# Optimization experiments

Hardware: AMD Instinct MI355X
Metric: run time of the kernel (lower is better)

Reference implementation:

```python
import jax, jax.numpy as jnp
import numpy as np

WIN = 15
BINS = 32
ALPHA = 0.9
LAM1 = 0.5
LAM2 = 0.5


def _tmedian(x, axis):
    # torch-style median: k-th smallest with k=(n-1)//2 (lower middle), keepdims
    n = x.shape[axis]
    s = jnp.sort(x, axis=axis)
    return jnp.take(s, jnp.array([(n - 1) // 2]), axis=axis)


def _box_sum_1d(x, k, axis):
    # sliding-window sum (zero padding) via cumsum / integral image
    p = k // 2
    L = x.shape[axis]
    c = jnp.cumsum(x, axis=axis)
    pad = [(0, 0)] * x.ndim
    pad[axis] = (1, 0)
    c = jnp.pad(c, pad)
    i = jnp.arange(L)
    hi = jnp.clip(i + p + 1, 0, L)
    lo = jnp.clip(i - p, 0, L)
    return jnp.take(c, hi, axis=axis) - jnp.take(c, lo, axis=axis)


def _counts_1d(L, k, dtype):
    p = k // 2
    i = jnp.arange(L)
    return (jnp.clip(i + p + 1, 0, L) - jnp.clip(i - p, 0, L)).astype(dtype)


def box_avg(x, k):
    # avg_pool2d(stride=1, padding=k//2, count_include_pad=False) on [B,C,H,W]
    s = _box_sum_1d(_box_sum_1d(x, k, 2), k, 3)
    c = _counts_1d(x.shape[2], k, x.dtype)[:, None] * _counts_1d(x.shape[3], k, x.dtype)[None, :]
    return s / c


def avg3(x):
    # avg_pool2d(k=3, stride=1, pad=1, count_include_pad=True)
    return _box_sum_1d(_box_sum_1d(x, 3, 2), 3, 3) / 9.0


def _softplus(x):
    t = jnp.log1p(jnp.exp(-jnp.abs(x)))
    return jnp.where(x >= 0, x + t, t)


def _conv3(x, k):
    return jax.lax.conv_general_dilated(x, k, (1, 1), ((1, 1), (1, 1)),
                                        dimension_numbers=('NCHW', 'OIHW', 'NCHW'))


def _forward(lab, a_rand):
    B, _, H, W = lab.shape
    N = H * W
    f32 = lab.dtype
    L = lab[:, 0:1]
    a = lab[:, 1:2]
    b = lab[:, 2:3]
    kx = jnp.array([[-1, 0, 1], [-2, 0, 2], [-1, 0, 1]], f32).reshape(1, 1, 3, 3)
    ky = jnp.array([[-1, -2, -1], [0, 0, 0], [1, 2, 1]], f32).reshape(1, 1, 3, 3)
    gx = _conv3(L, kx)
    gy = _conv3(L, ky)
    E = avg3(gx * gx) + avg3(gy * gy)           # structure-tensor trace
    S = jnp.sqrt(a * a + b * b + 1e-8)           # chroma
    Xf = jnp.concatenate([E, S], 1).reshape(B, 2, N).transpose(0, 2, 1)   # [B,N,2]
    yf = L.reshape(B, 1, N).transpose(0, 2, 1)                            # [B,N,1]
    XtX = jnp.einsum('bni,bnj->bij', Xf, Xf)
    XtY = jnp.einsum('bni,bnj->bij', Xf, yf)
    beta = jnp.linalg.solve(XtX + 1e-6 * jnp.eye(2, dtype=f32), XtY)[..., 0]  # [B,2]
    pred = beta[:, 0][:, None, None, None] * E + beta[:, 1][:, None, None, None] * S
    L_perp = L - pred
    # robust scale + whitening of [L_perp, E, S]
    X3f = jnp.concatenate([L_perp, E, S], 1).reshape(B, 3, N).transpose(0, 2, 1)  # [B,N,3]
    med = _tmedian(X3f, 1)
    mad = _tmedian(jnp.abs(X3f - med), 1) * 1.4826 + 1e-8
    Xz = (X3f - med) / mad
    diff = Xz - Xz.mean(1, keepdims=True)
    cov = jnp.einsum('bni,bnj->bij', diff, diff) / N
    e, V = jnp.linalg.eigh(jnp.maximum(cov, 1e-8))
    Wwh = jnp.einsum('bij,bj,bkj->bik', V, 1.0 / jnp.sqrt(e), V)
    Xw = diff @ Wwh                                                       # [B,N,3]
    # 128-way random-projection kurtosis search
    an = a_rand / (jnp.linalg.norm(a_rand, axis=-1, keepdims=True) + 1e-12)
    z = jnp.einsum('bni,bti->bnt', Xw, an)                                # [B,N,128]
    zc = z - z.mean(1, keepdims=True)
    m2 = (zc ** 2).mean(1) + 1e-12
    m4 = (zc ** 4).mean(1)
    kurt = m4 / (m2 * m2) - 3.0
    best = jnp.argmax(jnp.abs(kurt), axis=1)
    a_star = jnp.take_along_axis(an, best[:, None, None], axis=1)[:, 0]   # [B,3]
    z_best = jnp.einsum('bni,bi->bn', Xw, a_star)                         # [B,N]
    # 1-D 2-component GMM, 10 EM steps
    K = 2
    q25 = jnp.quantile(z_best, 0.25, axis=1)
    q75 = jnp.quantile(z_best, 0.75, axis=1)
    mu = jnp.stack([q25, q75], 1)[:, None, :]   # [B,1,K]
    var = jnp.ones((B, 1, K), f32)
    pi = jnp.full((B, 1, K), 0.5, f32)
    x1 = z_best[:, :, None]                      # [B,N,1]
    R = jnp.zeros((B, N, K), f32)
    for _ in range(10):
        logp = (-0.5 * ((x1 - mu) ** 2 / (var + 1e-6))
                - 0.5 * jnp.log(var + 1e-6) + jnp.log(pi + 1e-8))
        R = jnp.exp(jax.nn.log_softmax(logp, axis=2))
        Nk = R.sum(1, keepdims=True)             # [B,1,K]
        mu = (R * x1).sum(1, keepdims=True) / (Nk + 1e-8)
        var = (R * (x1 - mu) ** 2).sum(1, keepdims=True) / (Nk + 1e-8) + 1e-6
        pi = Nk / N
    R_alpha = R ** ALPHA
    R_alpha = R_alpha / (R_alpha.sum(2, keepdims=True) + 1e-8)
    rk_maps = R_alpha.transpose(0, 2, 1).reshape(B, K, 1, H, W)
    # per-cluster weighted Mahalanobis distance in [L_perp,E,S] space
    eye3 = jnp.eye(3, dtype=f32)
    Dk = []
    for k in range(K):
        w = R_alpha[:, :, k]
        Wsum = w.sum(1, keepdims=True) + 1e-8
        mu_k = jnp.einsum('bn,bni->bi', w, X3f) / Wsum
        Xm = X3f - mu_k[:, None, :]
        cov_k = jnp.einsum('bn,bni,bnj->bij', w, Xm, Xm) / Wsum[..., None] + 1e-6 * eye3
        inv_k = jnp.linalg.inv(cov_k)
        Dk.append(jnp.sqrt(jnp.einsum('bni,bij,bnj->bn', Xm, inv_k, Xm) + 1e-8))
    Dk = jnp.stack(Dk, 2)                        # [B,N,K]
    Rtemp = jax.nn.softmax(jnp.log(R_alpha + 1e-8), axis=2)
    D_M = (Rtemp * Dk).sum(2).reshape(B, 1, H, W)
    # local luminance anomaly (box-filtered weighted mean/std)
    Z_LLA = []
    for k in range(K):
        rk = rk_maps[:, k]
        den = box_avg(rk, WIN) + 1e-8
        mu_b = box_avg(rk * L_perp, WIN) / den
        var_b = jnp.maximum(box_avg(rk * L_perp ** 2, WIN) / den - mu_b ** 2, 1e-8)
        lla = jnp.abs(L_perp - mu_b) / (jnp.sqrt(var_b) + 1e-8)
        v = lla.reshape(B, 1, N)
        mv = _tmedian(v, 2)
        mdv = _tmedian(jnp.abs(v - mv), 2) * 1.4826 + 1e-8
        Z_LLA.append(((v - mv) / mdv).reshape(B, 1, H, W))
    # global-vs-local histogram distance (GLD)
    Lmin = L_perp.min(axis=(2, 3), keepdims=True)
    Lmax = L_perp.max(axis=(2, 3), keepdims=True)
    Lnorm = jnp.clip((L_perp - Lmin) / (Lmax - Lmin + 1e-8), 0, 1)
    idx = jnp.clip((Lnorm * BINS).astype(jnp.int32), 0, BINS - 1)[:, 0]   # [B,H,W]
    onehot = jax.nn.one_hot(idx, BINS, dtype=f32).transpose(0, 3, 1, 2)   # [B,bins,H,W]
    Z_GLD = []
    for k in range(K):
        rk = rk_maps[:, k]
        w_hist = onehot * rk
        g_hist = w_hist.reshape(B, BINS, N).sum(-1)
        g_hist = g_hist / (g_hist.sum(1, keepdims=True) + 1e-8)
        g_cdf = jnp.cumsum(g_hist, 1)
        loc_cdf = jnp.cumsum(box_avg(w_hist, WIN), 1) / (box_avg(rk, WIN) + 1e-8)
        GLD = jnp.abs(loc_cdf - g_cdf[:, :, None, None]).sum(1) / BINS    # [B,H,W]
        v = GLD.reshape(B, N)
        mv = _tmedian(v, 1)                                              # [B,1]
        mdv = _tmedian(jnp.abs(v - mv), 1) * 1.4826 + 1e-8
        Z_GLD.append(((GLD - mv[:, :, None]) / mdv[:, :, None])[:, None])
    gamma = jnp.ones_like(L_perp)
    for k in range(K):
        gamma = gamma + rk_maps[:, k] * (LAM1 * _softplus(Z_LLA[k]) + LAM2 * _softplus(Z_GLD[k]))
    # structural decorrelation term over [E,S]
    ES = jnp.concatenate([E, S], 1).reshape(B, 2, N).transpose(0, 2, 1)
    med2 = _tmedian(ES, 1)
    mad2 = _tmedian(jnp.abs(ES - med2), 1) * 1.4826 + 1e-8
    ESz = (ES - med2) / mad2
    d = ESz - ESz.mean(1, keepdims=True)
    cov2 = jnp.einsum('bni,bnj->bij', d, d) / N + 1e-6 * jnp.eye(2, dtype=f32)
    inv2 = jnp.linalg.inv(cov2)
    d2 = jnp.einsum('bni,bij,bnj->bn', d, inv2, d).reshape(B, 1, H, W)
    R_struct = jnp.exp(-0.5 * d2)
    L_anom = jnp.maximum(D_M * gamma * (1.0 - R_struct), 0.0)
    flat = L_anom.reshape(B, -1)
    q1 = jnp.quantile(flat, 0.01, axis=1).reshape(B, 1, 1, 1)
    q9 = jnp.quantile(flat, 0.99, axis=1).reshape(B, 1, 1, 1)
    L_anom_norm = jnp.clip((L_anom - q1) / (q9 - q1 + 1e-8), 0, 1)
    return L_perp, L_anom_norm


def setup_inputs() -> dict:
    key = jax.random.key(0)
    k1, k2 = jax.random.split(key)
    return {
        'batch_lab_raw': jax.random.normal(k1, (2, 3, 384, 384), jnp.float32),
        'a_rand': jax.random.normal(k2, (2, 128, 3), jnp.float32),
    }


def reference(batch_lab_raw, a_rand):
    return _forward(batch_lab_raw, a_rand)
```

## Files before the change

kernel.cpp:

```cpp
#include <hip/hip_runtime.h>
#include <math.h>

#define HH 384
#define WW 384
#define NPIX (HH*WW)
#define NB 2
#define BN (NB*NPIX)
#define NT 128
#define NBINS 32
#define MEDRANK ((NPIX-1)/2)
#define RB 72
#define RB2 288
#define SEL_BLK 64
#define KDG 8
#define KSEG 16

#define A_BETA 0
#define A_XZ   16
#define A_ES   40
#define A_DK   56
#define A_GMM  128
#define A_ZTOT 272
#define A_GHIST 288
#define A_KURT 512

#define F_BETA 0
#define F_X3   8
#define F_MEAN 24
#define F_WWH  32
#define F_ASTAR 828
#define F_ZBQ  868
#define F_DKINV 880
#define F_LLA  918
#define F_GLD  924
#define F_ESI  940
#define F_LAQ  952
#define F_GCDF 968
#define F_MMS_MIN 1280
#define F_MMS_MAX 1408


__device__ __forceinline__ double waveSum(double v){
#pragma unroll
  for(int o=32;o;o>>=1) v += __shfl_down(v,o,64);
  return v;
}
__device__ __forceinline__ unsigned f2u(float f){
  unsigned u = __float_as_uint(f);
  return (u & 0x80000000u) ? ~u : (u | 0x80000000u);
}
__device__ __forceinline__ float u2f(unsigned u){
  return __uint_as_float((u & 0x80000000u) ? (u ^ 0x80000000u) : ~u);
}
__device__ __forceinline__ float sp(float x){
  float t = log1pf(expf(-fabsf(x)));
  return x >= 0.f ? x + t : t;
}

struct SelBatch {
  const float* src[8];
  int rank[8];
  int fslot[8];
  int nt;
  int medmad;
};

__device__ void pickN(const unsigned* hp, int nb, int rank, unsigned& sel, int& nrank){
  __shared__ unsigned s_cum[256];
  __shared__ unsigned s_res[2];
  int tid = threadIdx.x;
  int base = tid*8;
  unsigned loc[8]; unsigned tsum=0;
#pragma unroll
  for(int j=0;j<8;j++){ unsigned v=(base+j<nb)?hp[base+j]:0u; loc[j]=v; tsum+=v; }
  s_cum[tid]=tsum;
  __syncthreads();
  for(int o=1;o<256;o<<=1){
    unsigned t=(tid>=o)?s_cum[tid-o]:0u;
    __syncthreads();
    s_cum[tid]+=t;
    __syncthreads();
  }
  unsigned cum=s_cum[tid], ex=cum-tsum;
  if(tsum>0u && (unsigned)rank>=ex && (unsigned)rank<cum){
    int rr=rank-(int)ex; unsigned bsel=0;
#pragma unroll
    for(int j=0;j<8;j++){ if((unsigned)rr<loc[j]){ bsel=(unsigned)(base+j); break; } rr-=(int)loc[j]; }
    s_res[0]=bsel; s_res[1]=(unsigned)rr;
  }
  __syncthreads();
  sel=s_res[0]; nrank=(int)s_res[1];
  __syncthreads();
}

__global__ void k_zero(double* A, float* F, unsigned* T, unsigned* H){
  int i = blockIdx.x*256 + threadIdx.x;
  if(i < 2048) A[i] = 0.0;
  if(i < 4096){
    unsigned* U = (unsigned*)F;
    unsigned v = 0u;
    if(i>=F_MMS_MIN && i<F_MMS_MIN+64) v = 0xFFFFFFFFu;
    U[i] = v;
  }
  if(i < 512) T[i] = 0u;
  for(int j=i; j<240*2048; j+=65536) H[j]=0u;
}

__global__ __launch_bounds__(256) void k_selp(SelBatch sb, unsigned* Hh, unsigned* T,
                                              float* F, int bid, int stage, int p){
  int task = blockIdx.x / SEL_BLK;
  int blk  = blockIdx.x % SEL_BLK;
  unsigned* meta = T + 384 + task*8;
  float center = (stage==1) ? __uint_as_float(meta[4]) : 0.f;
  unsigned pre = (p==2) ? 0u : meta[stage*2];
  __shared__ unsigned lh[2048];
  for(int j=threadIdx.x;j<2048;j+=256) lh[j]=0u;
  __syncthreads();
  const float* src = sb.src[task];
  for(int i=blk*256+threadIdx.x; i<NPIX; i+=SEL_BLK*256){
    float v = src[i];
    if(stage) v = fabsf(v-center);
    unsigned u = f2u(v);
    unsigned bin; bool ok;
    if(p==2){ bin = u>>21; ok = true; }
    else if(p==1){ bin = (u>>10)&2047u; ok = ((u>>21)==pre); }
    else { bin = u&1023u; ok = ((u>>10)==pre); }
    if(ok) atomicAdd(&lh[bin],1u);
  }
  __syncthreads();
  unsigned* hp = Hh + (size_t)(((bid*8+task)*2+stage)*3 + (2-p))*2048;
  for(int j=threadIdx.x;j<2048;j+=256){ unsigned c=lh[j]; if(c) atomicAdd(hp+j,c); }
  __shared__ int s_last;
  __syncthreads();
  if(threadIdx.x==0){
    __threadfence();
    s_last = (atomicAdd(&T[16+bid*64+task*8+stage*4+(2-p)],1u) == (unsigned)(SEL_BLK-1));
  }
  __syncthreads();
  if(!s_last) return;
  int r = (p==2) ? sb.rank[task] : (int)meta[stage*2+1];
  int nb = (p==0) ? 1024 : 2048;
  unsigned sel; int nr;
  pickN(hp, nb, r, sel, nr);
  if(threadIdx.x==0){
    if(p==2){ meta[stage*2]=sel; meta[stage*2+1]=(unsigned)nr; }
    else if(p==1){ meta[stage*2]=(pre<<11)|sel; meta[stage*2+1]=(unsigned)nr; }
    else {
      float val = u2f((pre<<10)|sel);
      if(stage==0){
        if(sb.medmad) meta[4]=__float_as_uint(val);
        else F[sb.fslot[task]]=val;
      } else {
        F[sb.fslot[task]]   = __uint_as_float(meta[4]);
        F[sb.fslot[task]+1] = val*1.4826f + 1e-8f;
      }
    }
  }
}

__device__ void quad_from_stats(double N0,double Sx0,double Sxx0,double Sxt,double Sxxt,
                                float& qa,float& qb,float& qc){
  double Nt=(double)NPIX;
  double N1=Nt-N0, Sx1=Sxt-Sx0, Sxx1=Sxxt-Sxx0;
  double mu0=Sx0/(N0+1e-8), mu1=Sx1/(N1+1e-8);
  double v0=(Sxx0-2.0*mu0*Sx0+mu0*mu0*N0)/(N0+1e-8)+1e-6;
  double v1=(Sxx1-2.0*mu1*Sx1+mu1*mu1*N1)/(N1+1e-8)+1e-6;
  double p0=N0/Nt, p1=N1/Nt;
  double c0=-0.5*log(v0+1e-6)+log(p0+1e-8);
  double c1=-0.5*log(v1+1e-6)+log(p1+1e-8);
  double iv0=0.5/(v0+1e-6), iv1=0.5/(v1+1e-6);
  qa=(float)(iv0-iv1);
  qb=(float)(2.0*(iv1*mu1-iv0*mu0));
  qc=(float)(iv0*mu0*mu0-iv1*mu1*mu1+c1-c0);
}
__device__ void quad_init(const float* F,int b,float& qa,float& qb,float& qc){
  const float* z = F + F_ZBQ + b*4;
  double h25 = 0.25*(double)(NPIX-1); double f25 = h25 - floor(h25);
  double h75 = 0.75*(double)(NPIX-1); double f75 = h75 - floor(h75);
  double mu0 = (double)z[0] + f25*((double)z[1]-(double)z[0]);
  double mu1 = (double)z[2] + f75*((double)z[3]-(double)z[2]);
  double iv = 0.5/(1.0+1e-6);
  qa = 0.f;
  qb = (float)(2.0*iv*(mu1-mu0));
  qc = (float)(iv*(mu0*mu0-mu1*mu1));
}

__global__ __launch_bounds__(256) void k_sobel(const float* lab, float* S, float* E){
  int bx = blockIdx.x % 24, by = (blockIdx.x/24) % 24, b = blockIdx.x/576;
  __shared__ float Lt[20][21];
  __shared__ float G[18][19];
  const float* Lb = lab + b*3*NPIX;
  int ox = bx*16, oy = by*16;
  for(int i=threadIdx.x; i<400; i+=256){
    int lx=i%20, ly=i/20;
    int gx_=ox-2+lx, gy_=oy-2+ly;
    Lt[ly][lx] = (gx_<0||gx_>=WW||gy_<0||gy_>=HH)?0.f:Lb[gy_*WW+gx_];
  }
  __syncthreads();
  for(int i=threadIdx.x; i<324; i+=256){
    int lx=i%18, ly=i/18;
    int px=lx+1, py=ly+1;
    int gxp=ox-2+px, gyp=oy-2+py;
    float g=0.f;
    if(gxp>=0&&gxp<WW&&gyp>=0&&gyp<HH){
      float gx = -Lt[py-1][px-1]+Lt[py-1][px+1] -2.f*Lt[py][px-1]+2.f*Lt[py][px+1] -Lt[py+1][px-1]+Lt[py+1][px+1];
      float gy = -Lt[py-1][px-1]-2.f*Lt[py-1][px]-Lt[py-1][px+1] +Lt[py+1][px-1]+2.f*Lt[py+1][px]+Lt[py+1][px+1];
      g = gx*gx+gy*gy;
    }
    G[ly][lx]=g;
  }
  __syncthreads();
  int tx = threadIdx.x%16, ty = threadIdx.x/16;
  float s=0;
#pragma unroll
  for(int dy=0;dy<3;dy++)
#pragma unroll
    for(int dx=0;dx<3;dx++) s += G[ty+dy][tx+dx];
  int n = (oy+ty)*WW + ox+tx;
  E[b*NPIX+n] = s*(1.f/9.f);
  float av=Lb[NPIX+n], bv=Lb[2*NPIX+n];
  S[b*NPIX+n] = sqrtf(av*av+bv*bv+1e-8f);
}

__global__ void k_beta_red(const float* E,const float* S,const float* lab,double* A,
                           float* F, unsigned* T){
  int b = blockIdx.x / RB, blk = blockIdx.x % RB;
  double s[5]={0,0,0,0,0};
  for(int n = blk*256 + threadIdx.x; n < NPIX; n += RB*256){
    float e=E[b*NPIX+n], ss=S[b*NPIX+n], l=lab[b*3*NPIX+n];
    s[0]+=(double)e*e; s[1]+=(double)e*ss; s[2]+=(double)ss*ss;
    s[3]+=(double)e*l; s[4]+=(double)ss*l;
  }
  __shared__ double red[4][5];
  int wave=threadIdx.x>>6, lane=threadIdx.x&63;
#pragma unroll
  for(int q=0;q<5;q++){
    s[q]=waveSum(s[q]);
    if(lane==0) red[wave][q]=s[q];
  }
  __syncthreads();
  if(threadIdx.x<5){
    double v = red[0][threadIdx.x]+red[1][threadIdx.x]+red[2][threadIdx.x]+red[3][threadIdx.x];
    atomicAdd(&A[A_BETA+b*5+threadIdx.x], v);
  }
  __shared__ int s_last;
  __syncthreads();
  if(threadIdx.x==0){
    __threadfence();
    s_last = (atomicAdd(&T[0],1u) == (unsigned)(NB*RB-1));
  }
  __syncthreads();
  if(!s_last || threadIdx.x) return;
  for(int bb=0;bb<NB;bb++){
    double EE=A[A_BETA+bb*5],ES=A[A_BETA+bb*5+1],SS=A[A_BETA+bb*5+2],EL=A[A_BETA+bb*5+3],SL=A[A_BETA+bb*5+4];
    double a00=EE+1e-6, a01=ES, a11=SS+1e-6;
    double det=a00*a11-a01*a01;
    F[F_BETA+bb*2]  =(float)(( a11*EL - a01*SL)/det);
    F[F_BETA+bb*2+1]=(float)((-a01*EL + a00*SL)/det);
  }
}

__global__ void k_lperp(const float* lab,const float* E,const float* S,const float* F,float* out0){
  int i = blockIdx.x*256 + threadIdx.x;
  int b=i/NPIX, n=i%NPIX;
  float v = lab[b*3*NPIX+n] - F[F_BETA+b*2]*E[i] - F[F_BETA+b*2+1]*S[i];
  out0[i] = v;
  unsigned u = f2u(v);
  unsigned mn=u, mx=u;
#pragma unroll
  for(int o=32;o;o>>=1){
    unsigned a = __shfl_down(mn,o,64); mn = (a<mn)?a:mn;
    unsigned c = __shfl_down(mx,o,64); mx = (c>mx)?c:mx;
  }
  __shared__ unsigned rmn[4], rmx[4];
  int wave=threadIdx.x>>6, lane=threadIdx.x&63;
  if(lane==0){ rmn[wave]=mn; rmx[wave]=mx; }
  __syncthreads();
  if(threadIdx.x==0){
    unsigned m0 = rmn[0]; unsigned m1 = rmx[0];
    for(int w=1;w<4;w++){ if(rmn[w]<m0)m0=rmn[w]; if(rmx[w]>m1)m1=rmx[w]; }
    unsigned* U = (unsigned*)F;
    int slot = blockIdx.x & 31;
    atomicMin(&U[F_MMS_MIN+b*32+slot], m0);
    atomicMax(&U[F_MMS_MAX+b*32+slot], m1);
  }
}

__global__ void k_xz_red(const float* Lp,const float* E,const float* S,float* F,double* A,
                         unsigned* T){
  int b = blockIdx.x / RB, blk = blockIdx.x % RB;
  const float* M = F + F_X3 + b*6;
  double s[9]={0,0,0,0,0,0,0,0,0};
  for(int n = blk*256 + threadIdx.x; n < NPIX; n += RB*256){
    float z0=(Lp[b*NPIX+n]-M[0])/M[1];
    float z1=(E [b*NPIX+n]-M[2])/M[3];
    float z2=(S [b*NPIX+n]-M[4])/M[5];
    s[0]+=z0; s[1]+=z1; s[2]+=z2;
    s[3]+=(double)z0*z0; s[4]+=(double)z0*z1; s[5]+=(double)z0*z2;
    s[6]+=(double)z1*z1; s[7]+=(double)z1*z2; s[8]+=(double)z2*z2;
  }
  __shared__ double red[4][9];
  int wave=threadIdx.x>>6, lane=threadIdx.x&63;
#pragma unroll
  for(int q=0;q<9;q++){
    s[q]=waveSum(s[q]);
    if(lane==0) red[wave][q]=s[q];
  }
  __syncthreads();
  if(threadIdx.x<9){
    double v = red[0][threadIdx.x]+red[1][threadIdx.x]+red[2][threadIdx.x]+red[3][threadIdx.x];
    atomicAdd(&A[A_XZ+b*9+threadIdx.x], v);
  }
  __shared__ int s_last;
  __syncthreads();
  if(threadIdx.x==0){
    __threadfence();
    s_last = (atomicAdd(&T[1],1u) == (unsigned)(NB*RB-1));
  }
  __syncthreads();
  if(!s_last) return;
  int bb = threadIdx.x;
  if(bb>=NB) return;
  const double* ss = A + A_XZ + bb*9;
  double inv = 1.0/(double)NPIX;
  double m0=ss[0]*inv, m1=ss[1]*inv, m2=ss[2]*inv;
  double a[3][3];
  a[0][0]=fmax(ss[3]*inv-m0*m0,1e-8);
  a[0][1]=a[1][0]=fmax(ss[4]*inv-m0*m1,1e-8);
  a[0][2]=a[2][0]=fmax(ss[5]*inv-m0*m2,1e-8);
  a[1][1]=fmax(ss[6]*inv-m1*m1,1e-8);
  a[1][2]=a[2][1]=fmax(ss[7]*inv-m1*m2,1e-8);
  a[2][2]=fmax(ss[8]*inv-m2*m2,1e-8);
  double V[3][3]={{1,0,0},{0,1,0},{0,0,1}};
  for(int sweep=0;sweep<40;sweep++){
    for(int pp=0;pp<3;pp++){
      int p = (pp==2)?1:0;
      int q = (pp==0)?1:2;
      double apq=a[p][q];
      if(fabs(apq)<1e-30) continue;
      double theta=(a[q][q]-a[p][p])/(2.0*apq);
      double t=((theta>=0)?1.0:-1.0)/(fabs(theta)+sqrt(1.0+theta*theta));
      double c=1.0/sqrt(1.0+t*t), sn=t*c;
      for(int k2=0;k2<3;k2++){ double akp=a[k2][p],akq=a[k2][q];
        a[k2][p]=c*akp-sn*akq; a[k2][q]=sn*akp+c*akq; }
      for(int k2=0;k2<3;k2++){ double apk=a[p][k2],aqk=a[q][k2];
        a[p][k2]=c*apk-sn*aqk; a[q][k2]=sn*apk+c*aqk; }
      for(int k2=0;k2<3;k2++){ double vkp=V[k2][p],vkq=V[k2][q];
        V[k2][p]=c*vkp-sn*vkq; V[k2][q]=sn*vkp+c*vkq; }
    }
  }
  double is0=1.0/sqrt(a[0][0]), is1=1.0/sqrt(a[1][1]), is2=1.0/sqrt(a[2][2]);
  for(int i=0;i<3;i++) for(int j=0;j<3;j++){
    double w = V[i][0]*is0*V[j][0] + V[i][1]*is1*V[j][1] + V[i][2]*is2*V[j][2];
    F[F_WWH + bb*9 + i*3 + j] = (float)w;
  }
  F[F_MEAN+bb*3]=(float)m0; F[F_MEAN+bb*3+1]=(float)m1; F[F_MEAN+bb*3+2]=(float)m2;
}

__global__ void k_xw(const float* Lp,const float* E,const float* S,const float* F,
                     float* Xw,int* idxP){
  __shared__ float s_mn, s_mx;
  int i = blockIdx.x*256 + threadIdx.x;
  int b=i/NPIX;
  if(threadIdx.x==0){
    const unsigned* U = (const unsigned*)F;
    unsigned mn=0xFFFFFFFFu, mx=0u;
    for(int s2=0;s2<32;s2++){
      unsigned a=U[F_MMS_MIN+b*32+s2]; if(a<mn)mn=a;
      unsigned c=U[F_MMS_MAX+b*32+s2]; if(c>mx)mx=c;
    }
    s_mn=u2f(mn); s_mx=u2f(mx);
  }
  __syncthreads();
  const float* M = F + F_X3 + b*6;
  float lp = Lp[i];
  float z0=(lp-M[0])/M[1];
  float z1=(E [i]-M[2])/M[3];
  float z2=(S [i]-M[4])/M[5];
  float d0=z0-F[F_MEAN+b*3], d1=z1-F[F_MEAN+b*3+1], d2=z2-F[F_MEAN+b*3+2];
  const float* Wm = F + F_WWH + b*9;
  Xw[3*(size_t)i  ]=d0*Wm[0]+d1*Wm[3]+d2*Wm[6];
  Xw[3*(size_t)i+1]=d0*Wm[1]+d1*Wm[4]+d2*Wm[7];
  Xw[3*(size_t)i+2]=d0*Wm[2]+d1*Wm[5]+d2*Wm[8];
  float ln = (lp-s_mn)/(s_mx-s_mn+1e-8f);
  ln = fminf(fmaxf(ln,0.f),1.f);
  int id = (int)(ln*32.f);
  idxP[i] = id>31?31:(id<0?0:id);
}

__global__ __launch_bounds__(256) void k_kurt(const float* Xw, const float* arand, double* A){
  int g = blockIdx.x;
  int b   = g / ((NT/KDG)*KSEG);
  int rem = g % ((NT/KDG)*KSEG);
  int dg  = rem / KSEG;
  int seg = rem % KSEG;
  float a0[KDG],a1[KDG],a2[KDG];
#pragma unroll
  for(int j=0;j<KDG;j++){
    const float* ar = arand + (b*NT+dg*KDG+j)*3;
    float q0=ar[0],q1=ar[1],q2=ar[2];
    float nrm=(float)(sqrt((double)q0*q0+(double)q1*q1+(double)q2*q2)+1e-12);
    a0[j]=q0/nrm; a1[j]=q1/nrm; a2[j]=q2/nrm;
  }
  const float* X = Xw + (size_t)b*NPIX*3;
  double s[KDG][4];
#pragma unroll
  for(int j=0;j<KDG;j++){ s[j][0]=0; s[j][1]=0; s[j][2]=0; s[j][3]=0; }
  const int cnt = NPIX/KSEG;
  int start = seg*cnt;
  for(int n=start+threadIdx.x; n<start+cnt; n+=256){
    const float* p = X + 3*(size_t)n;
    float x=p[0], y=p[1], z=p[2];
#pragma unroll
    for(int j=0;j<KDG;j++){
      float zz = fmaf(x,a0[j],fmaf(y,a1[j], z*a2[j]));
      float z2f = zz*zz;
      s[j][0]+=zz; s[j][1]+=z2f; s[j][2]+=z2f*zz; s[j][3]+=(double)z2f*z2f;
    }
  }
  __shared__ double red[4][KDG*4];
  int wave=threadIdx.x>>6, lane=threadIdx.x&63;
#pragma unroll
  for(int j=0;j<KDG;j++)
#pragma unroll
    for(int m=0;m<4;m++){
      double v=waveSum(s[j][m]);
      if(lane==0) red[wave][j*4+m]=v;
    }
  __syncthreads();
  if(threadIdx.x<KDG*4){
    double v = red[0][threadIdx.x]+red[1][threadIdx.x]+red[2][threadIdx.x]+red[3][threadIdx.x];
    int j=threadIdx.x>>2, m=threadIdx.x&3;
    atomicAdd(&A[A_KURT + (size_t)(b*NT+dg*KDG+j)*4 + m], v);
  }
}
__global__ void k_kurt_pick(const double* A, const float* arand, float* F){
  int b = blockIdx.x;
  int t = threadIdx.x;
  __shared__ float ak[NT];
  const double* K = A + A_KURT + (size_t)(b*NT+t)*4;
  double inv=1.0/(double)NPIX;
  double mean=K[0]*inv, M2=K[1]*inv, M3=K[2]*inv, M4=K[3]*inv;
  double m2 = M2 - mean*mean + 1e-12;
  double m4 = M4 - 4.0*mean*M3 + 6.0*mean*mean*M2 - 3.0*mean*mean*mean*mean;
  ak[t] = (float)fabs(m4/(m2*m2) - 3.0);
  __syncthreads();
  if(t==0){
    int best=0; float bv=ak[0];
    for(int j=1;j<NT;j++) if(ak[j]>bv){bv=ak[j];best=j;}
    const float* ar = arand + (b*NT+best)*3;
    double nrm = sqrt((double)ar[0]*ar[0]+(double)ar[1]*ar[1]+(double)ar[2]*ar[2])+1e-12;
    F[F_ASTAR+b*3]  =(float)(ar[0]/nrm);
    F[F_ASTAR+b*3+1]=(float)(ar[1]/nrm);
    F[F_ASTAR+b*3+2]=(float)(ar[2]/nrm);
  }
}
__global__ void k_zbest(const float* Xw,const float* F,float* zb,double* A){
  int i = blockIdx.x*256 + threadIdx.x;
  int b=i/NPIX;
  const float* p = Xw + 3*(size_t)i;
  float v = p[0]*F[F_ASTAR+b*3] + p[1]*F[F_ASTAR+b*3+1] + p[2]*F[F_ASTAR+b*3+2];
  zb[i]=v;
  double s0=waveSum((double)v), s1=waveSum((double)v*v);
  __shared__ double red[4][2];
  int wave=threadIdx.x>>6, lane=threadIdx.x&63;
  if(lane==0){ red[wave][0]=s0; red[wave][1]=s1; }
  __syncthreads();
  if(threadIdx.x<2){
    double v2 = red[0][threadIdx.x]+red[1][threadIdx.x]+red[2][threadIdx.x]+red[3][threadIdx.x];
    atomicAdd(&A[A_ZTOT+b*2+threadIdx.x], v2);
  }
}

__global__ __launch_bounds__(256) void k_gmm_red(const float* zb, const float* F, double* A, int it){
  __shared__ float Q[3];
  __shared__ double red[4][3];
  int b = blockIdx.x / RB2, blk = blockIdx.x % RB2;
  if(threadIdx.x==0){
    float qa,qb,qc;
    if(it==0) quad_init(F,b,qa,qb,qc);
    else {
      const double* g = A + A_GMM + (it-1)*8 + b*4;
      quad_from_stats(g[0],g[1],g[2],A[A_ZTOT+b*2],A[A_ZTOT+b*2+1],qa,qb,qc);
    }
    Q[0]=qa;Q[1]=qb;Q[2]=qc;
  }
  __syncthreads();
  float qa=Q[0],qb=Q[1],qc=Q[2];
  double s0=0,s1=0,s2=0;
  for(int n = blk*256 + threadIdx.x; n < NPIX; n += RB2*256){
    float x = zb[b*NPIX+n];
    float f = fmaf(fmaf(qa,x,qb),x,qc);
    float r0 = 1.f/(1.f+expf(f));
    float rx = r0*x;
    s0+=r0; s1+=rx; s2+=(double)rx*x;
  }
  int wave=threadIdx.x>>6, lane=threadIdx.x&63;
  s0=waveSum(s0); s1=waveSum(s1); s2=waveSum(s2);
  if(lane==0){ red[wave][0]=s0; red[wave][1]=s1; red[wave][2]=s2; }
  __syncthreads();
  if(threadIdx.x<3){
    double v = red[0][threadIdx.x]+red[1][threadIdx.x]+red[2][threadIdx.x]+red[3][threadIdx.x];
    atomicAdd(&A[A_GMM+it*8+b*4+threadIdx.x], v);
  }
}

__global__ void k_ralpha(const float* zb, float* F, double* A, const int* idxP,
                         float* Ra0, float* Ra1, unsigned* T){
  __shared__ float h0[NBINS], h1[NBINS];
  __shared__ float Q[3];
  if(threadIdx.x<NBINS){ h0[threadIdx.x]=0.f; h1[threadIdx.x]=0.f; }
  int i = blockIdx.x*256 + threadIdx.x;
  int b=i/NPIX;
  if(threadIdx.x==0){
    const double* g = A + A_GMM + 8*8 + b*4;
    float qa,qb,qc;
    quad_from_stats(g[0],g[1],g[2],A[A_ZTOT+b*2],A[A_ZTOT+b*2+1],qa,qb,qc);
    Q[0]=qa;Q[1]=qb;Q[2]=qc;
  }
  __syncthreads();
  float x = zb[i];
  float f = fmaf(fmaf(Q[0],x,Q[1]),x,Q[2]);
  float r0 = 1.f/(1.f+expf(f));
  float r1 = 1.f-r0;
  float ra0=powf(r0,0.9f), ra1=powf(r1,0.9f);
  float s=ra0+ra1+1e-8f;
  ra0/=s; ra1/=s;
  Ra0[i]=ra0; Ra1[i]=ra1;
  int id = idxP[i];
  atomicAdd(&h0[id], ra0);
  atomicAdd(&h1[id], ra1);
  __syncthreads();
  if(threadIdx.x<NBINS){
    if(h0[threadIdx.x]!=0.f) atomicAdd(&A[A_GHIST+(0*NB+b)*32+threadIdx.x], (double)h0[threadIdx.x]);
    if(h1[threadIdx.x]!=0.f) atomicAdd(&A[A_GHIST+(1*NB+b)*32+threadIdx.x], (double)h1[threadIdx.x]);
  }
  __shared__ int s_last;
  __syncthreads();
  if(threadIdx.x==0){
    __threadfence();
    s_last = (atomicAdd(&T[2],1u) == (unsigned)(BN/256-1));
  }
  __syncthreads();
  if(!s_last) return;
  int t = threadIdx.x;
  if(t>=4) return;
  const double* gh = A + A_GHIST + t*32;
  double sum=0;
  for(int j=0;j<NBINS;j++) sum += gh[j];
  double c=0;
  for(int j=0;j<NBINS;j++){
    c += gh[j]/(sum+1e-8);
    F[F_GCDF+t*32+j]=(float)c;
  }
}

__global__ void k_dk_red(const float* Lp,const float* E,const float* S,
                         const float* Ra0,const float* Ra1,double* A,float* F,unsigned* T){
  int b = blockIdx.x / RB, blk = blockIdx.x % RB;
  double s[20];
#pragma unroll
  for(int q=0;q<20;q++) s[q]=0;
  for(int n = blk*256 + threadIdx.x; n < NPIX; n += RB*256){
    int i=b*NPIX+n;
    double w0=Ra0[i], w1=Ra1[i];
    double x0=Lp[i], x1=E[i], x2=S[i];
    s[0]+=w0; s[1]+=w0*x0; s[2]+=w0*x1; s[3]+=w0*x2;
    s[4]+=w0*x0*x0; s[5]+=w0*x0*x1; s[6]+=w0*x0*x2; s[7]+=w0*x1*x1; s[8]+=w0*x1*x2; s[9]+=w0*x2*x2;
    s[10]+=w1; s[11]+=w1*x0; s[12]+=w1*x1; s[13]+=w1*x2;
    s[14]+=w1*x0*x0; s[15]+=w1*x0*x1; s[16]+=w1*x0*x2; s[17]+=w1*x1*x1; s[18]+=w1*x1*x2; s[19]+=w1*x2*x2;
  }
  __shared__ double red[4][20];
  int wave=threadIdx.x>>6, lane=threadIdx.x&63;
#pragma unroll
  for(int q=0;q<20;q++){
    s[q]=waveSum(s[q]);
    if(lane==0) red[wave][q]=s[q];
  }
  __syncthreads();
  if(threadIdx.x<20){
    double v = red[0][threadIdx.x]+red[1][threadIdx.x]+red[2][threadIdx.x]+red[3][threadIdx.x];
    atomicAdd(&A[A_DK+b*20+threadIdx.x], v);
  }
  __shared__ int s_last;
  __syncthreads();
  if(threadIdx.x==0){
    __threadfence();
    s_last = (atomicAdd(&T[3],1u) == (unsigned)(NB*RB-1));
  }
  __syncthreads();
  if(!s_last || threadIdx.x) return;
  for(int bb=0;bb<NB;bb++) for(int k=0;k<2;k++){
    const double* ss = A + A_DK + (bb*2+k)*10;
    double W0=ss[0], Ws=W0+1e-8;
    double mu0=ss[1]/Ws, mu1=ss[2]/Ws, mu2=ss[3]/Ws;
    double C00=(ss[4]-2.0*mu0*ss[1]+mu0*mu0*W0)/Ws + 1e-6;
    double C01=(ss[5]-mu0*ss[2]-mu1*ss[1]+mu0*mu1*W0)/Ws;
    double C02=(ss[6]-mu0*ss[3]-mu2*ss[1]+mu0*mu2*W0)/Ws;
    double C11=(ss[7]-2.0*mu1*ss[2]+mu1*mu1*W0)/Ws + 1e-6;
    double C12=(ss[8]-mu1*ss[3]-mu2*ss[2]+mu1*mu2*W0)/Ws;
    double C22=(ss[9]-2.0*mu2*ss[3]+mu2*mu2*W0)/Ws + 1e-6;
    double det = C00*(C11*C22-C12*C12) - C01*(C01*C22-C12*C02) + C02*(C01*C12-C11*C02);
    double id = 1.0/det;
    float* P = F + F_DKINV + (bb*2+k)*9;
    P[0]=(float)((C11*C22-C12*C12)*id);
    P[1]=(float)((C02*C12-C01*C22)*id);
    P[2]=(float)((C01*C12-C02*C11)*id);
    P[3]=(float)((C00*C22-C02*C02)*id);
    P[4]=(float)((C01*C02-C00*C12)*id);
    P[5]=(float)((C00*C11-C01*C01)*id);
    P[6]=(float)mu0; P[7]=(float)mu1; P[8]=(float)mu2;
  }
}
__global__ void k_dm(const float* Lp,const float* E,const float* S,
                     const float* Ra0,const float* Ra1,const float* F,float* DM){
  int i = blockIdx.x*256 + threadIdx.x; if(i>=BN) return;
  int b=i/NPIX;
  float x0=Lp[i], x1=E[i], x2=S[i];
  float D[2];
#pragma unroll
  for(int k=0;k<2;k++){
    const float* P = F + F_DKINV + (b*2+k)*9;
    float d0=x0-P[6], d1=x1-P[7], d2=x2-P[8];
    float q = d0*d0*P[0] + d1*d1*P[3] + d2*d2*P[5]
            + 2.f*(d0*d1*P[1] + d0*d2*P[2] + d1*d2*P[4]);
    D[k]=sqrtf(q+1e-8f);
  }
  float w0=Ra0[i]+1e-8f, w1=Ra1[i]+1e-8f;
  DM[i] = (w0*D[0]+w1*D[1])/(w0+w1);
}

__global__ __launch_bounds__(256) void k_lla(const float* rk, const float* Lp, float* tmpL){
  int bx = blockIdx.x % 24, by = (blockIdx.x/24) % 24, b = blockIdx.x/576;
  __shared__ float Rt[30][31], Lt[30][31];
  __shared__ float h0[30][17], h1[30][17], h2[30][17];
  int ox = bx*16, oy = by*16;
  const float* Rb = rk + (size_t)b*NPIX;
  const float* Lb = Lp + (size_t)b*NPIX;
  for(int i=threadIdx.x; i<900; i+=256){
    int lx=i%30, ly=i/30;
    int gx_=ox-7+lx, gy_=oy-7+ly;
    bool in = (gx_>=0&&gx_<WW&&gy_>=0&&gy_<HH);
    Rt[ly][lx]= in ? Rb[gy_*WW+gx_] : 0.f;
    Lt[ly][lx]= in ? Lb[gy_*WW+gx_] : 0.f;
  }
  __syncthreads();
  for(int i=threadIdx.x; i<480; i+=256){
    int j=i%16, r=i/16;
    float s0=0,s1=0,s2=0;
#pragma unroll
    for(int d=0;d<15;d++){
      float rr=Rt[r][j+d], ll=Lt[r][j+d];
      s0+=rr; float rl=rr*ll; s1+=rl; s2+=rl*ll;
    }
    h0[r][j]=s0; h1[r][j]=s1; h2[r][j]=s2;
  }
  __syncthreads();
  int tx=threadIdx.x%16, ty=threadIdx.x/16;
  float S0=0,S1=0,S2=0;
#pragma unroll
  for(int d=0;d<15;d++){ S0+=h0[ty+d][tx]; S1+=h1[ty+d][tx]; S2+=h2[ty+d][tx]; }
  int x=ox+tx, y=oy+ty;
  float cy = (float)((y+8<HH?y+8:HH)-(y-7>0?y-7:0));
  float cx = (float)((x+8<WW?x+8:WW)-(x-7>0?x-7:0));
  float cnt = cy*cx;
  float den = S0/cnt + 1e-8f;
  float mu  = (S1/cnt)/den;
  float var = fmaxf((S2/cnt)/den - mu*mu, 1e-8f);
  int n = y*WW+x;
  tmpL[b*NPIX+n] = fabsf(Lb[n]-mu)/(sqrtf(var)+1e-8f);
}

__global__ __launch_bounds__(256) void k_gldf(const float* rk, const int* idxP, const float* F,
                                              int k, float* tmpG){
  int bx = blockIdx.x % 24, by = (blockIdx.x/24) % 24, b = blockIdx.x/576;
  __shared__ float Rt[30][31];
  __shared__ unsigned char It[30][32];
  __shared__ float Hh[480*33];
  __shared__ float gc[NBINS];
  if(threadIdx.x<NBINS) gc[threadIdx.x]=F[F_GCDF+(k*NB+b)*32+threadIdx.x];
  int ox=bx*16, oy=by*16;
  const float* Rb = rk + (size_t)b*NPIX;
  const int* Ib = idxP + (size_t)b*NPIX;
  for(int i=threadIdx.x;i<900;i+=256){
    int lx=i%30, ly=i/30;
    int gx_=ox-7+lx, gy_=oy-7+ly;
    bool in = (gx_>=0&&gx_<WW&&gy_>=0&&gy_<HH);
    Rt[ly][lx] = in? Rb[gy_*WW+gx_] : 0.f;
    It[ly][lx] = in? (unsigned char)Ib[gy_*WW+gx_] : 0;
  }
  for(int i=threadIdx.x;i<480*33;i+=256) Hh[i]=0.f;
  __syncthreads();
  for(int i=threadIdx.x;i<480;i+=256){
    int j=i%16, r=i/16;
    float* my = Hh + i*33;
    for(int d=0;d<15;d++) my[It[r][j+d]] += Rt[r][j+d];
  }
  __syncthreads();
  int tx=threadIdx.x%16, ty=threadIdx.x/16;
  float vs[32];
  float tot=0;
#pragma unroll
  for(int bin=0;bin<NBINS;bin++){
    float s=0;
#pragma unroll
    for(int d=0;d<15;d++) s += Hh[((ty+d)*16+tx)*33+bin];
    vs[bin]=s; tot+=s;
  }
  int x=ox+tx, y=oy+ty;
  float cy = (float)((y+8<HH?y+8:HH)-(y-7>0?y-7:0));
  float cx = (float)((x+8<WW?x+8:WW)-(x-7>0?x-7:0));
  float cnt = cy*cx;
  float den = tot/cnt + 1e-8f;
  float cs=0, acc=0;
#pragma unroll
  for(int bin=0;bin<NBINS;bin++){
    cs += vs[bin];
    acc += fabsf((cs/cnt)/den - gc[bin]);
  }
  tmpG[b*NPIX + y*WW + x] = acc*(1.f/32.f);
}

__global__ void k_gamma(const float* tmpL,const float* tmpG,const float* rk,const float* F,
                        float* gamma,int first){
  int i = blockIdx.x*256 + threadIdx.x; if(i>=BN) return;
  int b=i/NPIX;
  float zl=(tmpL[i]-F[F_LLA+b*2])/F[F_LLA+b*2+1];
  float zg=(tmpG[i]-F[F_GLD+b*2])/F[F_GLD+b*2+1];
  float c = rk[i]*(0.5f*sp(zl)+0.5f*sp(zg));
  gamma[i] = first ? 1.0f + c : gamma[i] + c;
}

__global__ void k_es_red(const float* E,const float* S,float* F,double* A,unsigned* T){
  int b = blockIdx.x / RB, blk = blockIdx.x % RB;
  const float* M = F + F_X3 + b*6;
  double s[5]={0,0,0,0,0};
  for(int n = blk*256 + threadIdx.x; n < NPIX; n += RB*256){
    float z0=(E[b*NPIX+n]-M[2])/M[3];
    float z1=(S[b*NPIX+n]-M[4])/M[5];
    s[0]+=z0; s[1]+=z1; s[2]+=(double)z0*z0; s[3]+=(double)z0*z1; s[4]+=(double)z1*z1;
  }
  __shared__ double red[4][5];
  int wave=threadIdx.x>>6, lane=threadIdx.x&63;
#pragma unroll
  for(int q=0;q<5;q++){
    s[q]=waveSum(s[q]);
    if(lane==0) red[wave][q]=s[q];
  }
  __syncthreads();
  if(threadIdx.x<5){
    double v = red[0][threadIdx.x]+red[1][threadIdx.x]+red[2][threadIdx.x]+red[3][threadIdx.x];
    atomicAdd(&A[A_ES+b*5+threadIdx.x], v);
  }
  __shared__ int s_last;
  __syncthreads();
  if(threadIdx.x==0){
    __threadfence();
    s_last = (atomicAdd(&T[4],1u) == (unsigned)(NB*RB-1));
  }
  __syncthreads();
  if(!s_last || threadIdx.x) return;
  for(int bb=0;bb<NB;bb++){
    const double* ss = A + A_ES + bb*5;
    double inv=1.0/(double)NPIX;
    double m0=ss[0]*inv, m1=ss[1]*inv;
    double c00=ss[2]*inv - m0*m0 + 1e-6;
    double c01=ss[3]*inv - m0*m1;
    double c11=ss[4]*inv - m1*m1 + 1e-6;
    double det=c00*c11-c01*c01;
    float* P = F + F_ESI + bb*5;
    P[0]=(float)m0; P[1]=(float)m1;
    P[2]=(float)(c11/det); P[3]=(float)(-c01/det); P[4]=(float)(c00/det);
  }
}
__global__ void k_lanom(const float* E,const float* S,const float* DM,const float* gamma,
                        const float* F,float* La){
  int i = blockIdx.x*256 + threadIdx.x; if(i>=BN) return;
  int b=i/NPIX;
  const float* M = F + F_X3 + b*6;
  const float* P = F + F_ESI + b*5;
  float z0=(E[i]-M[2])/M[3];
  float z1=(S[i]-M[4])/M[5];
  float d0=z0-P[0], d1=z1-P[1];
  float d2 = d0*d0*P[2] + 2.f*d0*d1*P[3] + d1*d1*P[4];
  float Rs = expf(-0.5f*d2);
  La[i] = fmaxf(DM[i]*gamma[i]*(1.f-Rs), 0.f);
}
__global__ void k_out2(const float* La, const float* F, float* out){
  int i = blockIdx.x*256 + threadIdx.x; if(i>=BN) return;
  int b=i/NPIX;
  const float* v = F + F_LAQ + b*4;
  double h1 = 0.01*(double)(NPIX-1); double f1 = h1 - floor(h1);
  double h9 = 0.99*(double)(NPIX-1); double f9 = h9 - floor(h9);
  float q1 = (float)((double)v[0] + f1*((double)v[1]-(double)v[0]));
  float q9 = (float)((double)v[2] + f9*((double)v[3]-(double)v[2]));
  float r = (La[i]-q1)/(q9-q1+1e-8f);
  out[BN + i] = fminf(fmaxf(r,0.f),1.f);
}

static void run_sel(const SelBatch& sb, unsigned* H, unsigned* T, float* F, int bid, hipStream_t s){
  for(int p=2;p>=0;--p) k_selp<<<sb.nt*SEL_BLK,256,0,s>>>(sb,H,T,F,bid,0,p);
  if(sb.medmad) for(int p=2;p>=0;--p) k_selp<<<sb.nt*SEL_BLK,256,0,s>>>(sb,H,T,F,bid,1,p);
}

extern "C" void kernel_launch(void* const* d_in, const int* in_sizes, int n_in,
                              void* d_out, int out_size, void* d_ws, size_t ws_size,
                              hipStream_t stream){
  (void)in_sizes; (void)n_in; (void)out_size; (void)ws_size;
  const float* lab   = (const float*)d_in[0];
  const float* arand = (const float*)d_in[1];
  float* out = (float*)d_out;
  char* wsb = (char*)d_ws;
  double* A = (double*)wsb;
  float*  F = (float*)(wsb + 16384);
  unsigned* T = (unsigned*)(wsb + 32768);
  unsigned* H = (unsigned*)(wsb + 65536);
  float* planes = (float*)(wsb + (size_t)4*1024*1024);
  float* E    = planes;
  float* S    = planes + (size_t)BN;
  float* tA   = planes + (size_t)2*BN;
  float* tmpL = planes + (size_t)5*BN;
  float* tmpG = planes + (size_t)6*BN;
  float* Xw   = planes + (size_t)7*BN;
  float* zb   = planes + (size_t)10*BN;
  float* Ra0  = planes + (size_t)11*BN;
  float* Ra1  = planes + (size_t)12*BN;
  float* DM   = planes + (size_t)13*BN;
  float* gamma= planes + (size_t)14*BN;
  int*   idxP = (int*)(planes + (size_t)16*BN);

  const int GBN = BN/256;

  k_zero<<<256,256,0,stream>>>(A,F,T,H);
  k_sobel<<<NB*576,256,0,stream>>>(lab,S,E);
  k_beta_red<<<NB*RB,256,0,stream>>>(E,S,lab,A,F,T);
  k_lperp<<<GBN,256,0,stream>>>(lab,E,S,F,out);

  SelBatch sbX; sbX.nt=6; sbX.medmad=1;
  for(int b=0;b<NB;b++){
    sbX.src[b*3+0]=out+(size_t)b*NPIX; sbX.src[b*3+1]=E+(size_t)b*NPIX; sbX.src[b*3+2]=S+(size_t)b*NPIX;
    for(int ch=0;ch<3;ch++){ sbX.rank[b*3+ch]=MEDRANK; sbX.fslot[b*3+ch]=F_X3+(b*3+ch)*2; }
  }
  run_sel(sbX,H,T,F,0,stream);

  k_xz_red<<<NB*RB,256,0,stream>>>(out,E,S,F,A,T);
  k_xw<<<GBN,256,0,stream>>>(out,E,S,F,Xw,idxP);
  k_kurt<<<NB*(NT/KDG)*KSEG,256,0,stream>>>(Xw,arand,A);
  k_kurt_pick<<<NB,128,0,stream>>>(A,arand,F);
  k_zbest<<<GBN,256,0,stream>>>(Xw,F,zb,A);

  SelBatch sbZ; sbZ.nt=8; sbZ.medmad=0;
  {
    int rr[4]={36863,36864,110591,110592};
    for(int b=0;b<NB;b++) for(int ri=0;ri<4;ri++){
      int t=b*4+ri;
      sbZ.src[t]=zb+(size_t)b*NPIX; sbZ.rank[t]=rr[ri]; sbZ.fslot[t]=F_ZBQ+b*4+ri;
    }
  }
  run_sel(sbZ,H,T,F,1,stream);

  for(int it=0; it<9; ++it)
    k_gmm_red<<<NB*RB2,256,0,stream>>>(zb,F,A,it);
  k_ralpha<<<GBN,256,0,stream>>>(zb,F,A,idxP,Ra0,Ra1,T);
  k_dk_red<<<NB*RB,256,0,stream>>>(out,E,S,Ra0,Ra1,A,F,T);
  k_dm<<<GBN,256,0,stream>>>(out,E,S,Ra0,Ra1,F,DM);

  SelBatch sbC; sbC.nt=4; sbC.medmad=1;
  for(int b=0;b<NB;b++){
    sbC.src[b]  =tmpL+(size_t)b*NPIX; sbC.rank[b]  =MEDRANK; sbC.fslot[b]  =F_LLA+b*2;
    sbC.src[2+b]=tmpG+(size_t)b*NPIX; sbC.rank[2+b]=MEDRANK; sbC.fslot[2+b]=F_GLD+b*2;
  }

  for(int k=0;k<2;k++){
    const float* Rk = k ? Ra1 : Ra0;
    k_lla<<<NB*576,256,0,stream>>>(Rk,out,tmpL);
    k_gldf<<<NB*576,256,0,stream>>>(Rk,idxP,F,k,tmpG);
    run_sel(sbC,H,T,F,2+k,stream);
    k_gamma<<<GBN,256,0,stream>>>(tmpL,tmpG,Rk,F,gamma,k==0?1:0);
  }

  k_es_red<<<NB*RB,256,0,stream>>>(E,S,F,A,T);
  k_lanom<<<GBN,256,0,stream>>>(E,S,DM,gamma,F,tA);

  SelBatch sbL; sbL.nt=8; sbL.medmad=0;
  {
    int rr[4]={1474,1475,145980,145981};
    for(int b=0;b<NB;b++) for(int ri=0;ri<4;ri++){
      int t=b*4+ri;
      sbL.src[t]=tA+(size_t)b*NPIX; sbL.rank[t]=rr[ri]; sbL.fslot[t]=F_LAQ+b*4+ri;
    }
  }
  run_sel(sbL,H,T,F,4,stream);

  k_out2<<<GBN,256,0,stream>>>(tA,F,out);
}
```

Baseline: 703.3 us.

## Batch both mixture components into single local-stat, selection and gamma launches

Merges the two per-component passes of k_lla/k_gldf into single double-size grids, runs one median/MAD selection over all 8 planes instead of two 4-plane runs, and computes gamma for both components in one kernel. The kurtosis pick is folded into k_kurt with a last-block atomic counter, which removes a separate launch. The GLD shared histogram is transposed to bin-major layout without padding to change bank access patterns. These cut launch count and serialization but use more workspace and require the T[5] counter and the selection slot indices to stay consistent.

```diff
diff --git a/kernel.cpp b/kernel.cpp
--- a/kernel.cpp
+++ b/kernel.cpp
@@ -31,8 +31,7 @@
 #define F_ASTAR 828
 #define F_ZBQ  868
 #define F_DKINV 880
-#define F_LLA  918
-#define F_GLD  924
+#define F_CM   918
 #define F_ESI  940
 #define F_LAQ  952
 #define F_GCDF 968
@@ -388,7 +387,8 @@
   idxP[i] = id>31?31:(id<0?0:id);
 }
 
-__global__ __launch_bounds__(256) void k_kurt(const float* Xw, const float* arand, double* A){
+__global__ __launch_bounds__(256) void k_kurt(const float* Xw, const float* arand,
+                                              double* A, float* F, unsigned* T){
   int g = blockIdx.x;
   int b   = g / ((NT/KDG)*KSEG);
   int rem = g % ((NT/KDG)*KSEG);
@@ -433,28 +433,37 @@
     int j=threadIdx.x>>2, m=threadIdx.x&3;
     atomicAdd(&A[A_KURT + (size_t)(b*NT+dg*KDG+j)*4 + m], v);
   }
-}
-__global__ void k_kurt_pick(const double* A, const float* arand, float* F){
-  int b = blockIdx.x;
-  int t = threadIdx.x;
-  __shared__ float ak[NT];
-  const double* K = A + A_KURT + (size_t)(b*NT+t)*4;
-  double inv=1.0/(double)NPIX;
-  double mean=K[0]*inv, M2=K[1]*inv, M3=K[2]*inv, M4=K[3]*inv;
-  double m2 = M2 - mean*mean + 1e-12;
-  double m4 = M4 - 4.0*mean*M3 + 6.0*mean*mean*M2 - 3.0*mean*mean*mean*mean;
-  ak[t] = (float)fabs(m4/(m2*m2) - 3.0);
-  __syncthreads();
-  if(t==0){
-    int best=0; float bv=ak[0];
-    for(int j=1;j<NT;j++) if(ak[j]>bv){bv=ak[j];best=j;}
-    const float* ar = arand + (b*NT+best)*3;
+  __shared__ int s_last;
+  __syncthreads();
+  if(threadIdx.x==0){
+    __threadfence();
+    s_last = (atomicAdd(&T[5],1u) == (unsigned)(NB*(NT/KDG)*KSEG-1));
+  }
+  __syncthreads();
+  if(!s_last) return;
+  __shared__ float ak[NB*NT];
+  {
+    int tid=threadIdx.x;
+    const double* K = A + A_KURT + (size_t)tid*4;
+    double inv=1.0/(double)NPIX;
+    double mean=K[0]*inv, M2=K[1]*inv, M3=K[2]*inv, M4=K[3]*inv;
+    double m2 = M2 - mean*mean + 1e-12;
+    double m4 = M4 - 4.0*mean*M3 + 6.0*mean*mean*M2 - 3.0*mean*mean*mean*mean;
+    ak[tid] = (float)fabs(m4/(m2*m2) - 3.0);
+  }
+  __syncthreads();
+  if(threadIdx.x<NB){
+    int bb=threadIdx.x;
+    int best=0; float bv=ak[bb*NT];
+    for(int j=1;j<NT;j++){ float v=ak[bb*NT+j]; if(v>bv){bv=v;best=j;} }
+    const float* ar = arand + (bb*NT+best)*3;
     double nrm = sqrt((double)ar[0]*ar[0]+(double)ar[1]*ar[1]+(double)ar[2]*ar[2])+1e-12;
-    F[F_ASTAR+b*3]  =(float)(ar[0]/nrm);
-    F[F_ASTAR+b*3+1]=(float)(ar[1]/nrm);
-    F[F_ASTAR+b*3+2]=(float)(ar[2]/nrm);
-  }
-}
+    F[F_ASTAR+bb*3]  =(float)(ar[0]/nrm);
+    F[F_ASTAR+bb*3+1]=(float)(ar[1]/nrm);
+    F[F_ASTAR+bb*3+2]=(float)(ar[2]/nrm);
+  }
+}
+
 __global__ void k_zbest(const float* Xw,const float* F,float* zb,double* A){
   int i = blockIdx.x*256 + threadIdx.x;
   int b=i/NPIX;
@@ -630,8 +639,12 @@
   DM[i] = (w0*D[0]+w1*D[1])/(w0+w1);
 }
 
-__global__ __launch_bounds__(256) void k_lla(const float* rk, const float* Lp, float* tmpL){
-  int bx = blockIdx.x % 24, by = (blockIdx.x/24) % 24, b = blockIdx.x/576;
+__global__ __launch_bounds__(256) void k_lla(const float* Ra0, const float* Ra1,
+                                             const float* Lp, float* tmpL){
+  int kk = blockIdx.x / (NB*576);
+  int inner = blockIdx.x % (NB*576);
+  int bx = inner % 24, by = (inner/24) % 24, b = inner/576;
+  const float* rk = kk ? Ra1 : Ra0;
   __shared__ float Rt[30][31], Lt[30][31];
   __shared__ float h0[30][17], h1[30][17], h2[30][17];
   int ox = bx*16, oy = by*16;
@@ -668,17 +681,20 @@
   float mu  = (S1/cnt)/den;
   float var = fmaxf((S2/cnt)/den - mu*mu, 1e-8f);
   int n = y*WW+x;
-  tmpL[b*NPIX+n] = fabsf(Lb[n]-mu)/(sqrtf(var)+1e-8f);
-}
-
-__global__ __launch_bounds__(256) void k_gldf(const float* rk, const int* idxP, const float* F,
-                                              int k, float* tmpG){
-  int bx = blockIdx.x % 24, by = (blockIdx.x/24) % 24, b = blockIdx.x/576;
+  tmpL[(size_t)kk*BN + b*NPIX+n] = fabsf(Lb[n]-mu)/(sqrtf(var)+1e-8f);
+}
+
+__global__ __launch_bounds__(256) void k_gldf(const float* Ra0, const float* Ra1,
+                                              const int* idxP, const float* F, float* tmpG){
+  int kk = blockIdx.x / (NB*576);
+  int inner = blockIdx.x % (NB*576);
+  int bx = inner % 24, by = (inner/24) % 24, b = inner/576;
+  const float* rk = kk ? Ra1 : Ra0;
   __shared__ float Rt[30][31];
   __shared__ unsigned char It[30][32];
-  __shared__ float Hh[480*33];
+  __shared__ float Hh[32*480];
   __shared__ float gc[NBINS];
-  if(threadIdx.x<NBINS) gc[threadIdx.x]=F[F_GCDF+(k*NB+b)*32+threadIdx.x];
+  if(threadIdx.x<NBINS) gc[threadIdx.x]=F[F_GCDF+(kk*NB+b)*32+threadIdx.x];
   int ox=bx*16, oy=by*16;
   const float* Rb = rk + (size_t)b*NPIX;
   const int* Ib = idxP + (size_t)b*NPIX;
@@ -689,12 +705,11 @@
     Rt[ly][lx] = in? Rb[gy_*WW+gx_] : 0.f;
     It[ly][lx] = in? (unsigned char)Ib[gy_*WW+gx_] : 0;
   }
-  for(int i=threadIdx.x;i<480*33;i+=256) Hh[i]=0.f;
+  for(int i=threadIdx.x;i<32*480;i+=256) Hh[i]=0.f;
   __syncthreads();
   for(int i=threadIdx.x;i<480;i+=256){
     int j=i%16, r=i/16;
-    float* my = Hh + i*33;
-    for(int d=0;d<15;d++) my[It[r][j+d]] += Rt[r][j+d];
+    for(int d=0;d<15;d++) Hh[(int)It[r][j+d]*480 + i] += Rt[r][j+d];
   }
   __syncthreads();
   int tx=threadIdx.x%16, ty=threadIdx.x/16;
@@ -704,7 +719,7 @@
   for(int bin=0;bin<NBINS;bin++){
     float s=0;
 #pragma unroll
-    for(int d=0;d<15;d++) s += Hh[((ty+d)*16+tx)*33+bin];
+    for(int d=0;d<15;d++) s += Hh[bin*480 + (ty+d)*16+tx];
     vs[bin]=s; tot+=s;
   }
   int x=ox+tx, y=oy+ty;
@@ -718,17 +733,24 @@
     cs += vs[bin];
     acc += fabsf((cs/cnt)/den - gc[bin]);
   }
-  tmpG[b*NPIX + y*WW + x] = acc*(1.f/32.f);
-}
-
-__global__ void k_gamma(const float* tmpL,const float* tmpG,const float* rk,const float* F,
-                        float* gamma,int first){
+  tmpG[(size_t)kk*BN + b*NPIX + y*WW + x] = acc*(1.f/32.f);
+}
+
+__global__ void k_gamma(const float* tmpL,const float* tmpG,const float* Ra0,const float* Ra1,
+                        const float* F,float* gamma){
   int i = blockIdx.x*256 + threadIdx.x; if(i>=BN) return;
   int b=i/NPIX;
-  float zl=(tmpL[i]-F[F_LLA+b*2])/F[F_LLA+b*2+1];
-  float zg=(tmpG[i]-F[F_GLD+b*2])/F[F_GLD+b*2+1];
-  float c = rk[i]*(0.5f*sp(zl)+0.5f*sp(zg));
-  gamma[i] = first ? 1.0f + c : gamma[i] + c;
+  float g = 1.0f;
+#pragma unroll
+  for(int kk=0;kk<2;kk++){
+    const float* ML = F + F_CM + (kk*4 + 0 + b)*2;
+    const float* MG = F + F_CM + (kk*4 + 2 + b)*2;
+    float zl=(tmpL[(size_t)kk*BN+i]-ML[0])/ML[1];
+    float zg=(tmpG[(size_t)kk*BN+i]-MG[0])/MG[1];
+    float rk = kk ? Ra1[i] : Ra0[i];
+    g += rk*(0.5f*sp(zl)+0.5f*sp(zg));
+  }
+  gamma[i] = g;
 }
 
 __global__ void k_es_red(const float* E,const float* S,float* F,double* A,unsigned* T){
@@ -819,8 +841,8 @@
   float* E    = planes;
   float* S    = planes + (size_t)BN;
   float* tA   = planes + (size_t)2*BN;
-  float* tmpL = planes + (size_t)5*BN;
-  float* tmpG = planes + (size_t)6*BN;
+  float* tmpL = planes + (size_t)3*BN;
+  float* tmpG = planes + (size_t)5*BN;
   float* Xw   = planes + (size_t)7*BN;
   float* zb   = planes + (size_t)10*BN;
   float* Ra0  = planes + (size_t)11*BN;
@@ -845,8 +867,7 @@
 
   k_xz_red<<<NB*RB,256,0,stream>>>(out,E,S,F,A,T);
   k_xw<<<GBN,256,0,stream>>>(out,E,S,F,Xw,idxP);
-  k_kurt<<<NB*(NT/KDG)*KSEG,256,0,stream>>>(Xw,arand,A);
-  k_kurt_pick<<<NB,128,0,stream>>>(A,arand,F);
+  k_kurt<<<NB*(NT/KDG)*KSEG,256,0,stream>>>(Xw,arand,A,F,T);
   k_zbest<<<GBN,256,0,stream>>>(Xw,F,zb,A);
 
   SelBatch sbZ; sbZ.nt=8; sbZ.medmad=0;
@@ -865,19 +886,18 @@
   k_dk_red<<<NB*RB,256,0,stream>>>(out,E,S,Ra0,Ra1,A,F,T);
   k_dm<<<GBN,256,0,stream>>>(out,E,S,Ra0,Ra1,F,DM);
 
-  SelBatch sbC; sbC.nt=4; sbC.medmad=1;
-  for(int b=0;b<NB;b++){
-    sbC.src[b]  =tmpL+(size_t)b*NPIX; sbC.rank[b]  =MEDRANK; sbC.fslot[b]  =F_LLA+b*2;
-    sbC.src[2+b]=tmpG+(size_t)b*NPIX; sbC.rank[2+b]=MEDRANK; sbC.fslot[2+b]=F_GLD+b*2;
-  }
-
-  for(int k=0;k<2;k++){
-    const float* Rk = k ? Ra1 : Ra0;
-    k_lla<<<NB*576,256,0,stream>>>(Rk,out,tmpL);
-    k_gldf<<<NB*576,256,0,stream>>>(Rk,idxP,F,k,tmpG);
-    run_sel(sbC,H,T,F,2+k,stream);
-    k_gamma<<<GBN,256,0,stream>>>(tmpL,tmpG,Rk,F,gamma,k==0?1:0);
-  }
+  k_lla<<<2*NB*576,256,0,stream>>>(Ra0,Ra1,out,tmpL);
+  k_gldf<<<2*NB*576,256,0,stream>>>(Ra0,Ra1,idxP,F,tmpG);
+
+  SelBatch sbC; sbC.nt=8; sbC.medmad=1;
+  for(int kk=0;kk<2;kk++) for(int isG=0;isG<2;isG++) for(int b=0;b<NB;b++){
+    int t = kk*4 + isG*2 + b;
+    sbC.src[t] = (isG? tmpG: tmpL) + (size_t)kk*BN + (size_t)b*NPIX;
+    sbC.rank[t]=MEDRANK; sbC.fslot[t]=F_CM + t*2;
+  }
+  run_sel(sbC,H,T,F,2,stream);
+
+  k_gamma<<<GBN,256,0,stream>>>(tmpL,tmpG,Ra0,Ra1,F,gamma);
 
   k_es_red<<<NB*RB,256,0,stream>>>(E,S,F,A,T);
   k_lanom<<<GBN,256,0,stream>>>(E,S,DM,gamma,F,tA);
@@ -890,7 +910,7 @@
       sbL.src[t]=tA+(size_t)b*NPIX; sbL.rank[t]=rr[ri]; sbL.fslot[t]=F_LAQ+b*4+ri;
     }
   }
-  run_sel(sbL,H,T,F,4,stream);
+  run_sel(sbL,H,T,F,3,stream);
 
   k_out2<<<GBN,256,0,stream>>>(tA,F,out);
 }
```

Measured after the change: 642.1 us. 8.7% less time.
